# Kernel optimization log

Hardware: AMD Instinct MI355X
Metric: run time of the kernel (lower is better)

Reference implementation:

```python
import jax, jax.numpy as jnp
import numpy as np

N = 100_000   # nodes (batched over G graphs)
E = 3_200_000 # edges (avg degree 32)
G = 64        # graphs in the batch
IN_FEATS, H1, H3, NUM_CLASSES = 64, 64, 64, 2


def setup_inputs() -> dict:
    key = jax.random.key(0)
    ks = jax.random.split(key, 11)
    return {
        "in_feat": jax.random.normal(ks[0], (N, IN_FEATS), jnp.float32),
        "edge_weights": jax.random.uniform(ks[1], (E,), jnp.float32, 1e-3, 1.0),
        "W1": jax.random.normal(ks[2], (IN_FEATS, H1), jnp.float32) / np.sqrt(IN_FEATS),
        "b1": jnp.zeros((H1,), jnp.float32),
        "W2": jax.random.normal(ks[3], (H1, H3), jnp.float32) / np.sqrt(H1),
        "b2": jnp.zeros((H3,), jnp.float32),
        "Wc": jax.random.normal(ks[4], (H3, NUM_CLASSES), jnp.float32) / np.sqrt(H3),
        "bc": jnp.zeros((NUM_CLASSES,), jnp.float32),
        "edge_src": jax.random.randint(ks[5], (E,), 0, N, jnp.int32),
        "edge_dst": jax.random.randint(ks[6], (E,), 0, N, jnp.int32),
        "graph_ids": jnp.sort(jax.random.randint(ks[7], (N,), 0, G, jnp.int32)),
    }


def reference(in_feat, edge_weights, W1, b1, W2, b2, Wc, bc,
              edge_src, edge_dst, graph_ids):
    # EdgeWeightNorm(norm='right'): w_e / (sum of weights into dst(e))
    deg_w = jax.ops.segment_sum(edge_weights, edge_dst, num_segments=N)  # [N]
    nw = edge_weights / deg_w[edge_dst]                                  # [E]

    # unweighted in-degree used by SAGEConv 'gcn' aggregator
    deg = jax.ops.segment_sum(jnp.ones((E,), jnp.float32), edge_dst, num_segments=N)  # [N]

    def sage_gcn(h, W, b):
        # weighted neighbor sum: sum_e nw_e * h[src_e] scattered to dst
        msg = h[edge_src] * nw[:, None]                                  # [E, F]
        neigh = jax.ops.segment_sum(msg, edge_dst, num_segments=N)      # [N, F]
        h_neigh = (neigh + h) / (deg[:, None] + 1.0)                     # gcn: include self, /(deg+1)
        return h_neigh @ W + b                                           # fc_neigh + bias

    h = jax.nn.relu(sage_gcn(in_feat, W1, b1))
    h = jax.nn.relu(sage_gcn(h, W2, b2))

    # dgl.mean_nodes: per-graph mean of node features
    counts = jax.ops.segment_sum(jnp.ones((N,), jnp.float32), graph_ids, num_segments=G)
    hg = jax.ops.segment_sum(h, graph_ids, num_segments=G) / jnp.maximum(counts, 1.0)[:, None]

    return hg @ Wc + bc  # [G, num_classes]
```

## Files before the change

### kernel.cpp

```cpp
#include <hip/hip_runtime.h>
#include <hip/hip_fp16.h>


#define BK   1024
#define NB   128
#define CAPB 5120
#define CAPP 6144
#define SRC17 0x1FFFFu

__device__ __forceinline__ float readlane_f(float v, int l) {
    return __int_as_float(__builtin_amdgcn_readlane(__float_as_int(v), l));
}

__device__ __forceinline__ int2 ntload_i2(const int2* p) {
    unsigned long long r = __builtin_nontemporal_load((const unsigned long long*)p);
    return make_int2((int)(unsigned)(r & 0xffffffffull), (int)(unsigned)(r >> 32));
}

__device__ __forceinline__ void ntstore_f2(float2* p, float2 v) {
    union { float2 f; unsigned long long u; } c;
    c.f = v;
    __builtin_nontemporal_store(c.u, (unsigned long long*)p);
}

__global__ void k_cvt(const float4* __restrict__ x, uint2* __restrict__ xh, int n4) {
    int i = blockIdx.x * blockDim.x + threadIdx.x;
    if (i >= n4) return;
    float4 v = x[i];
    __half2 a = __floats2half2_rn(v.x, v.y);
    __half2 b = __floats2half2_rn(v.z, v.w);
    uint2 r;
    r.x = *(const unsigned*)&a;
    r.y = *(const unsigned*)&b;
    xh[i] = r;
}

__global__ __launch_bounds__(1024) void k_binB(
        const int* __restrict__ esrc, const int* __restrict__ edst,
        const float* __restrict__ ew, int* __restrict__ cursor,
        int2* __restrict__ bsw, int E, int CH) {
    __shared__ int h[BK];
    __shared__ int lcur[BK];
    const int tid = threadIdx.x;

    if (tid < BK) h[tid] = 0;
    __syncthreads();
    const int e0 = blockIdx.x * CH;
    const int e1 = min(E, e0 + CH);
    for (int e = e0 + tid; e < e1; e += 1024)
        atomicAdd(&h[edst[e] >> 7], 1);
    __syncthreads();
    if (tid < BK) {
        int c = h[tid];
        lcur[tid] = c ? atomicAdd(&cursor[tid], c) : 0;
    }
    __syncthreads();
    for (int e = e0 + tid; e < e1; e += 1024) {
        int d = edst[e];
        int b = d >> 7;
        int p = atomicAdd(&lcur[b], 1);
        if (p < CAPB)
            bsw[(size_t)b * CAPB + p] =
                make_int2(((d & 127) << 18) | esrc[e], __float_as_int(ew[e]));
    }
}

__global__ __launch_bounds__(512) void k_csrsort(
        const int2* __restrict__ bsw, const int* __restrict__ cursor,
        unsigned* __restrict__ csr, int* __restrict__ off, int* __restrict__ fill,
        int N) {
    __shared__ unsigned se[CAPP];
    __shared__ int cur[NB];
    __shared__ int pfx[NB];
    __shared__ int tot;
    const int b = blockIdx.x, tid = threadIdx.x;
    for (int i = tid; i < CAPP; i += 512) se[i] = 0u;
    if (tid < NB) cur[tid] = 0;
    __syncthreads();
    const int cnt = min(cursor[b], CAPB);
    const int2* __restrict__ eb = bsw + (size_t)b * CAPB;
    for (int i = tid; i < cnt; i += 512)
        atomicAdd(&cur[eb[i].x >> 18], 1);
    __syncthreads();
    int pc = 0;
    if (tid < NB) {
        int c0 = cur[tid & ~1], c1 = cur[tid | 1];
        pc = (max(c0, c1) + 7) & ~7;
        pfx[tid] = pc;
    }
    __syncthreads();
    for (int o = 1; o < NB; o <<= 1) {
        int t = 0;
        if (tid < NB && tid >= o) t = pfx[tid - o];
        __syncthreads();
        if (tid < NB) pfx[tid] += t;
        __syncthreads();
    }
    if (tid < NB) {
        int excl = pfx[tid] - pc;
        int node = b * NB + tid;
        if (node < N) { off[node] = b * CAPP + excl; fill[node] = cur[tid]; }
        cur[tid] = excl;
        if (tid == NB - 1) tot = min(pfx[tid], CAPP);
    }
    __syncthreads();
    for (int i = tid; i < cnt; i += 512) {
        int2 e = eb[i];
        int p = atomicAdd(&cur[e.x >> 18], 1);
        unsigned h15 = (unsigned)__half_as_ushort(
                           __float2half_rn(__int_as_float(e.y))) & 0x7FFFu;
        if (p < CAPP)
            se[p] = ((unsigned)e.x & SRC17) | (h15 << 17);
    }
    __syncthreads();
    const int T = tot;
    unsigned* __restrict__ cb = csr + (size_t)b * CAPP;
    for (int i = tid; i < T; i += 512) cb[i] = se[i];
}

__global__ void k_fill_pad(const int* __restrict__ esrc, const int* __restrict__ edst,
                           const float* __restrict__ ew, int* __restrict__ fill,
                           int2* __restrict__ csr, int E, int CAP) {
    int e = blockIdx.x * blockDim.x + threadIdx.x;
    if (e < E) {
        int d = edst[e];
        int p = atomicAdd(&fill[d], 1);
        if (p < CAP)
            csr[(size_t)d * CAP + p] = make_int2(esrc[e], __float_as_int(ew[e]));
    }
}

__global__ void k_cnt(const int* __restrict__ edst, int* __restrict__ cnt, int E) {
    int e = blockIdx.x * blockDim.x + threadIdx.x;
    if (e < E) atomicAdd(&cnt[edst[e]], 1);
}

__global__ void k_off(const int* __restrict__ cnt, int* __restrict__ off,
                      int* __restrict__ fill, int* __restrict__ cursor, int N) {
    int i    = blockIdx.x * blockDim.x + threadIdx.x;
    int lane = threadIdx.x & 63;
    int c    = (i < N) ? cnt[i] : 0;
    int pref = c;
    #pragma unroll
    for (int d = 1; d < 64; d <<= 1) {
        int t = __shfl_up(pref, d);
        if (lane >= d) pref += t;
    }
    int total = __shfl(pref, 63);
    int base  = 0;
    if (lane == 63) base = atomicAdd(cursor, total);
    base = __shfl(base, 63);
    if (i < N) {
        int p = base + pref - c;
        off[i]  = p;
        fill[i] = p;
    }
}

__global__ void k_fill(const int* __restrict__ esrc, const int* __restrict__ edst,
                       const float* __restrict__ ew, int* __restrict__ fill,
                       int2* __restrict__ csr, int E) {
    int e = blockIdx.x * blockDim.x + threadIdx.x;
    if (e < E) {
        int d = edst[e];
        int p = atomicAdd(&fill[d], 1);
        csr[p] = make_int2(esrc[e], __float_as_int(ew[e]));
    }
}

__global__ __launch_bounds__(256, 6) void k_agg_p(
        const unsigned* __restrict__ xh, const int* __restrict__ off,
        const int* __restrict__ cnt_arr, const unsigned* __restrict__ csr,
        float* __restrict__ agg, int N) {
    const int lane = threadIdx.x & 63;
    const int slot = lane >> 5;
    const int f8   = lane & 31;
    const int wq   = (blockIdx.x * blockDim.x + threadIdx.x) >> 6;
    const int nw   = (gridDim.x * blockDim.x) >> 6;
    const int npair = (N + 1) >> 1;

    for (int pr = wq; pr < npair; pr += nw) {
        const int  node  = 2 * pr + slot;
        const bool valid = node < N;
        const int  cnt_s = valid ? cnt_arr[node] : 0;
        const int  st_s  = valid ? off[node] : 0;
        const int  cA = __builtin_amdgcn_readlane(cnt_s, 0);
        const int  cB = __builtin_amdgcn_readlane(cnt_s, 32);
        const int  pc = (max(cA, cB) + 7) & ~7;

        float2 acc = {0.f, 0.f};
        float  sw  = 0.f;
        const unsigned* __restrict__ pS = csr + st_s;
        for (int k = 0; k < pc; k += 8) {
            uint4 e0 = *(const uint4*)(pS + k);
            uint4 e1 = *(const uint4*)(pS + k + 4);
            unsigned ev[8] = {e0.x, e0.y, e0.z, e0.w, e1.x, e1.y, e1.z, e1.w};
            float    w[8];
            unsigned u[8];
            #pragma unroll
            for (int t = 0; t < 8; ++t) {
                unsigned e = ev[t];
                w[t] = __half2float(__ushort_as_half((unsigned short)(e >> 17)));
                u[t] = xh[((e & SRC17) << 5) | (unsigned)f8];
            }
            #pragma unroll
            for (int t = 0; t < 8; ++t) {
                float2 v = __half22float2(*(const __half2*)&u[t]);
                acc.x = fmaf(w[t], v.x, acc.x);
                acc.y = fmaf(w[t], v.y, acc.y);
                sw += w[t];
            }
        }
        if (valid) {
            float invw = (sw > 0.f) ? (1.f / sw) : 0.f;
            float invd = 1.f / ((float)cnt_s + 1.f);
            unsigned us = xh[((unsigned)node << 5) | (unsigned)f8];
            float2 xs = __half22float2(*(const __half2*)&us);
            float2 hn;
            hn.x = (acc.x * invw + xs.x) * invd;
            hn.y = (acc.y * invw + xs.y) * invd;
            ntstore_f2(&((float2*)agg)[(size_t)node * 32 + f8], hn);
        }
    }
}

__global__ __launch_bounds__(256, 4) void k_agg_f(
        const unsigned* __restrict__ xh, const int* __restrict__ off,
        const int* __restrict__ cnt_arr, const int2* __restrict__ csr,
        float* __restrict__ agg, int N, int CAP) {
    const int lane   = threadIdx.x & 63;
    const int slot   = lane >> 5;
    const int f8     = lane & 31;
    const int wave   = (blockIdx.x * blockDim.x + threadIdx.x) >> 6;
    const int nwaves = (gridDim.x * blockDim.x) >> 6;

    int node  = wave;
    int cnt_p = 0, start_p = 0;
    if (node < N) {
        cnt_p   = cnt_arr[node];
        start_p = (CAP > 0) ? node * CAP : off[node];
        if (CAP > 0) cnt_p = min(cnt_p, CAP);
    }
    for (; node < N; node += nwaves) {
        const int cnt = cnt_p, start = start_p;
        int nn = node + nwaves;
        if (nn < N) {
            cnt_p   = cnt_arr[nn];
            start_p = (CAP > 0) ? nn * CAP : off[nn];
            if (CAP > 0) cnt_p = min(cnt_p, CAP);
        }
        int2 ee = make_int2(0, 0);
        if (lane < cnt) ee = ntload_i2(&csr[start + lane]);
        float2 acc0 = {0.f, 0.f}, acc1 = {0.f, 0.f};
        float  sw = 0.0f;
        for (int bk = 0; bk < cnt; bk += 64) {
            int   s_l = ee.x;
            float w_l = __int_as_float(ee.y);
            int2 en = make_int2(0, 0);
            int  rem = cnt - bk - 64;
            if (lane < rem) en = ntload_i2(&csr[start + bk + 64 + lane]);
            sw += w_l;
            #pragma unroll
            for (int half = 0; half < 2; ++half) {
                float    w[16];
                unsigned u[16];
                #pragma unroll
                for (int k = 0; k < 16; ++k) {
                    int idx = half * 32 + 2 * k + slot;
                    int s   = __shfl(s_l, idx);
                    w[k]    = __shfl(w_l, idx);
                    u[k]    = xh[(size_t)s * 32 + f8];
                }
                #pragma unroll
                for (int k = 0; k < 16; k += 2) {
                    float2 v0 = __half22float2(*(const __half2*)&u[k]);
                    float2 v1 = __half22float2(*(const __half2*)&u[k + 1]);
                    acc0.x = fmaf(w[k],     v0.x, acc0.x);
                    acc0.y = fmaf(w[k],     v0.y, acc0.y);
                    acc1.x = fmaf(w[k + 1], v1.x, acc1.x);
                    acc1.y = fmaf(w[k + 1], v1.y, acc1.y);
                }
            }
            ee = en;
        }
        acc0.x += acc1.x; acc0.y += acc1.y;
        acc0.x += __shfl_xor(acc0.x, 32);
        acc0.y += __shfl_xor(acc0.y, 32);
        #pragma unroll
        for (int mask = 1; mask <= 32; mask <<= 1) sw += __shfl_xor(sw, mask);
        float invw = (sw > 0.0f) ? (1.0f / sw) : 0.0f;
        float invd = 1.0f / ((float)cnt + 1.0f);
        if (lane < 32) {
            unsigned us = xh[(size_t)node * 32 + f8];
            float2 xs = __half22float2(*(const __half2*)&us);
            float2 hn;
            hn.x = (acc0.x * invw + xs.x) * invd;
            hn.y = (acc0.y * invw + xs.y) * invd;
            ntstore_f2(&((float2*)agg)[(size_t)node * 32 + f8], hn);
        }
    }
}

__global__ __launch_bounds__(256) void k_fc(
        const float* __restrict__ agg, const float* __restrict__ W,
        const float* __restrict__ b, __half* __restrict__ outh, int N) {
    const int lane   = threadIdx.x & 63;
    const int wave   = (blockIdx.x * blockDim.x + threadIdx.x) >> 6;
    const int nwaves = (gridDim.x * blockDim.x) >> 6;
    float wc[64];
    #pragma unroll
    for (int f = 0; f < 64; ++f) wc[f] = W[f * 64 + lane];
    const float bias = b[lane];
    for (int node = wave; node < N; node += nwaves) {
        float hn = agg[(size_t)node * 64 + lane];
        float o0 = bias, o1 = 0.f, o2 = 0.f, o3 = 0.f;
        #pragma unroll
        for (int f = 0; f < 64; f += 4) {
            o0 = fmaf(readlane_f(hn, f),     wc[f],     o0);
            o1 = fmaf(readlane_f(hn, f + 1), wc[f + 1], o1);
            o2 = fmaf(readlane_f(hn, f + 2), wc[f + 2], o2);
            o3 = fmaf(readlane_f(hn, f + 3), wc[f + 3], o3);
        }
        float o = fmaxf((o0 + o1) + (o2 + o3), 0.0f);
        outh[(size_t)node * 64 + lane] = __float2half_rn(o);
    }
}

__global__ __launch_bounds__(256) void k_fcpool(
        const float* __restrict__ agg, const float* __restrict__ W,
        const float* __restrict__ b, const int* __restrict__ gid,
        float* __restrict__ hg, float* __restrict__ cntg, int N) {
    const int lane   = threadIdx.x & 63;
    const int wave   = (blockIdx.x * blockDim.x + threadIdx.x) >> 6;
    const int nwaves = (gridDim.x * blockDim.x) >> 6;
    float wc[64];
    #pragma unroll
    for (int f = 0; f < 64; ++f) wc[f] = W[f * 64 + lane];
    const float bias = b[lane];
    const int per   = (N + nwaves - 1) / nwaves;
    const int start = wave * per;
    const int end   = min(N, start + per);
    if (start >= N) return;

    int   curg = -1;
    float acc  = 0.0f;
    int   c    = 0;
    for (int node = start; node < end; ++node) {
        float hn = agg[(size_t)node * 64 + lane];
        float o0 = bias, o1 = 0.f, o2 = 0.f, o3 = 0.f;
        #pragma unroll
        for (int f = 0; f < 64; f += 4) {
            o0 = fmaf(readlane_f(hn, f),     wc[f],     o0);
            o1 = fmaf(readlane_f(hn, f + 1), wc[f + 1], o1);
            o2 = fmaf(readlane_f(hn, f + 2), wc[f + 2], o2);
            o3 = fmaf(readlane_f(hn, f + 3), wc[f + 3], o3);
        }
        float o = fmaxf((o0 + o1) + (o2 + o3), 0.0f);
        int g = gid[node];
        if (g != curg) {
            if (c > 0) {
                atomicAdd(&hg[curg * 64 + lane], acc);
                if (lane == 0) atomicAdd(&cntg[curg], (float)c);
            }
            curg = g; acc = 0.0f; c = 0;
        }
        acc += o;
        ++c;
    }
    if (c > 0) {
        atomicAdd(&hg[curg * 64 + lane], acc);
        if (lane == 0) atomicAdd(&cntg[curg], (float)c);
    }
}

__global__ void k_out(const float* __restrict__ hg, const float* __restrict__ cntg,
                      const float* __restrict__ Wc, const float* __restrict__ bc,
                      float* __restrict__ out, int G) {
    int t = blockIdx.x * blockDim.x + threadIdx.x;
    if (t >= G * 2) return;
    int g = t >> 1, c = t & 1;
    float ct = fmaxf(cntg[g], 1.0f);
    float o  = bc[c];
    for (int f = 0; f < 64; ++f)
        o += (hg[g * 64 + f] / ct) * Wc[f * 2 + c];
    out[t] = o;
}

extern "C" void kernel_launch(void* const* d_in, const int* in_sizes, int n_in,
                              void* d_out, int out_size, void* d_ws, size_t ws_size,
                              hipStream_t stream) {
    const float* in_feat = (const float*)d_in[0];
    const float* ew      = (const float*)d_in[1];
    const float* W1      = (const float*)d_in[2];
    const float* b1      = (const float*)d_in[3];
    const float* W2      = (const float*)d_in[4];
    const float* b2      = (const float*)d_in[5];
    const float* Wc      = (const float*)d_in[6];
    const float* bc      = (const float*)d_in[7];
    const int*   esrc    = (const int*)d_in[8];
    const int*   edst    = (const int*)d_in[9];
    const int*   gid     = (const int*)d_in[10];

    const int E = in_sizes[1];
    const int N = in_sizes[10];
    const int G = out_size / 2;
    float* outp = (float*)d_out;

    auto alignup = [](size_t x) { return (x + 15) & ~(size_t)15; };
    char* base = (char*)d_ws;
    const int FC_BLK = 1024, AGG_BLK = 2048;
    const int n4 = N * 16;

    const int B   = (N + NB - 1) / NB;
    const int CHB = (E + 255) / 256;

    size_t zhdr  = ((size_t)G * 64 + G + BK) * 4;
    size_t o_off = alignup(zhdr);
    size_t o_fil = o_off + alignup((size_t)N * 4);
    size_t o_bsw = o_fil + alignup((size_t)N * 4);
    size_t o_csr = o_bsw + alignup((size_t)B * CAPB * 8);
    size_t o_t1  = o_csr + alignup((size_t)B * CAPP * 4);
    size_t o_t2  = o_t1 + alignup((size_t)N * 64 * 4);
    size_t o_xh  = o_t2 + alignup((size_t)N * 64 * 4);
    size_t o_th  = o_xh + alignup((size_t)N * 64 * 2);
    size_t needB = o_th + (size_t)N * 64 * 2;

    bool cap_ok = ((size_t)E / B) + 512 < CAPB && N <= (1 << 17);

    if (ws_size >= needB && B <= BK && cap_ok) {
        float*    hg     = (float*)base;
        float*    cntg   = hg + (size_t)G * 64;
        int*      cursor = (int*)(cntg + G);
        int*      off    = (int*)(base + o_off);
        int*      fill   = (int*)(base + o_fil);
        int2*     bsw    = (int2*)(base + o_bsw);
        unsigned* csr    = (unsigned*)(base + o_csr);
        float*    t1     = (float*)(base + o_t1);
        float*    t2     = (float*)(base + o_t2);
        unsigned* xh0    = (unsigned*)(base + o_xh);
        __half*   th1    = (__half*)(base + o_th);

        hipMemsetAsync(d_ws, 0, zhdr, stream);
        k_cvt    <<<(n4 + 255) / 256, 256, 0, stream>>>((const float4*)in_feat, (uint2*)xh0, n4);
        k_binB   <<<256, 1024, 0, stream>>>(esrc, edst, ew, cursor, bsw, E, CHB);
        k_csrsort<<<B, 512, 0, stream>>>(bsw, cursor, csr, off, fill, N);
        k_agg_p <<<AGG_BLK, 256, 0, stream>>>(xh0, off, fill, csr, t1, N);
        k_fc    <<<FC_BLK, 256, 0, stream>>>(t1, W1, b1, th1, N);
        k_agg_p <<<AGG_BLK, 256, 0, stream>>>((const unsigned*)th1, off, fill, csr, t2, N);
        k_fcpool<<<FC_BLK, 256, 0, stream>>>(t2, W2, b2, gid, hg, cntg, N);
        k_out   <<<1, 128, 0, stream>>>(hg, cntg, Wc, bc, outp, G);
        return;
    }

    const int CAP = 96;
    size_t hdr    = ((size_t)G * 64 + G + 1 + N) * 4;
    size_t needB2 = alignup(hdr) + alignup((size_t)N * CAP * 8)
                  + alignup((size_t)N * 64 * 4) * 2
                  + alignup((size_t)N * 64 * 2) * 2;
    if (ws_size >= needB2) {
        size_t o = 0;
        float* hg     = (float*)(base + o);
        float* cntg   = hg + (size_t)G * 64;
        int*   fill   = (int*)(cntg + G) + 1;
        o += alignup(hdr);
        int2*     csr = (int2*)(base + o);    o += alignup((size_t)N * CAP * 8);
        float*    t1  = (float*)(base + o);   o += alignup((size_t)N * 64 * 4);
        float*    t2  = (float*)(base + o);   o += alignup((size_t)N * 64 * 4);
        unsigned* xh0 = (unsigned*)(base + o); o += alignup((size_t)N * 64 * 2);
        __half*   th1 = (__half*)(base + o);

        hipMemsetAsync(d_ws, 0, hdr, stream);
        k_cvt     <<<(n4 + 255) / 256, 256, 0, stream>>>((const float4*)in_feat, (uint2*)xh0, n4);
        k_fill_pad<<<(E + 255) / 256, 256, 0, stream>>>(esrc, edst, ew, fill, csr, E, CAP);
        k_agg_f <<<AGG_BLK, 256, 0, stream>>>(xh0, (const int*)nullptr, fill, csr, t1, N, CAP);
        k_fc    <<<FC_BLK, 256, 0, stream>>>(t1, W1, b1, th1, N);
        k_agg_f <<<AGG_BLK, 256, 0, stream>>>((const unsigned*)th1, (const int*)nullptr, fill, csr, t2, N, CAP);
        k_fcpool<<<FC_BLK, 256, 0, stream>>>(t2, W2, b2, gid, hg, cntg, N);
        k_out   <<<1, 128, 0, stream>>>(hg, cntg, Wc, bc, outp, G);
        return;
    }

    {
        size_t o = 0;
        float* hg     = (float*)(base + o);
        float* cntg   = hg + (size_t)G * 64;
        int*   cursor = (int*)(cntg + G);
        int*   cnt    = cursor + 1;
        o += alignup(hdr);
        int*      off  = (int*)(base + o);    o += alignup((size_t)N * 4);
        int*      fill = (int*)(base + o);    o += alignup((size_t)N * 4);
        int2*     csr  = (int2*)(base + o);   o += alignup((size_t)E * 8);
        float*    t1   = (float*)(base + o);  o += alignup((size_t)N * 64 * 4);
        float*    t2   = (float*)(base + o);  o += alignup((size_t)N * 64 * 4);
        unsigned* xh0  = (unsigned*)(base + o); o += alignup((size_t)N * 64 * 2);
        __half*   th1  = (__half*)(base + o);

        hipMemsetAsync(d_ws, 0, hdr, stream);
        k_cvt <<<(n4 + 255) / 256, 256, 0, stream>>>((const float4*)in_feat, (uint2*)xh0, n4);
        k_cnt <<<(E + 255) / 256, 256, 0, stream>>>(edst, cnt, E);
        k_off <<<(N + 255) / 256, 256, 0, stream>>>(cnt, off, fill, cursor, N);
        k_fill<<<(E + 255) / 256, 256, 0, stream>>>(esrc, edst, ew, fill, csr, E);
        k_agg_f <<<AGG_BLK, 256, 0, stream>>>(xh0, off, cnt, csr, t1, N, 0);
        k_fc    <<<FC_BLK, 256, 0, stream>>>(t1, W1, b1, th1, N);
        k_agg_f <<<AGG_BLK, 256, 0, stream>>>((const unsigned*)th1, off, cnt, csr, t2, N, 0);
        k_fcpool<<<FC_BLK, 256, 0, stream>>>(t2, W2, b2, gid, hg, cntg, N);
        k_out   <<<1, 128, 0, stream>>>(hg, cntg, Wc, bc, outp, G);
    }
}
```

Measured before the change: 375.0 us.

## Fuse neighbor aggregation with dense layer and pooling per node block

Replaces the separate aggregation and FC kernels with two fused kernels. Each block aggregates 128 nodes into shared memory and then applies the 64x64 linear layer (plus ReLU, or plus the per-graph mean-pool atomics in layer two) directly. This removes the fp32 t1/t2 intermediate round trips through global memory and two kernel launches. In exchange, each block holds a 32KB shared tile and a 64-register weight column, which cuts occupancy for the latency-bound gather phase and removes the grid-stride load balancing.

```diff
diff --git a/kernel.cpp b/kernel.cpp
--- a/kernel.cpp
+++ b/kernel.cpp
@@ -118,71 +118,25 @@
     for (int i = tid; i < T; i += 512) cb[i] = se[i];
 }
 
-__global__ void k_fill_pad(const int* __restrict__ esrc, const int* __restrict__ edst,
-                           const float* __restrict__ ew, int* __restrict__ fill,
-                           int2* __restrict__ csr, int E, int CAP) {
-    int e = blockIdx.x * blockDim.x + threadIdx.x;
-    if (e < E) {
-        int d = edst[e];
-        int p = atomicAdd(&fill[d], 1);
-        if (p < CAP)
-            csr[(size_t)d * CAP + p] = make_int2(esrc[e], __float_as_int(ew[e]));
-    }
-}
-
-__global__ void k_cnt(const int* __restrict__ edst, int* __restrict__ cnt, int E) {
-    int e = blockIdx.x * blockDim.x + threadIdx.x;
-    if (e < E) atomicAdd(&cnt[edst[e]], 1);
-}
-
-__global__ void k_off(const int* __restrict__ cnt, int* __restrict__ off,
-                      int* __restrict__ fill, int* __restrict__ cursor, int N) {
-    int i    = blockIdx.x * blockDim.x + threadIdx.x;
-    int lane = threadIdx.x & 63;
-    int c    = (i < N) ? cnt[i] : 0;
-    int pref = c;
-    #pragma unroll
-    for (int d = 1; d < 64; d <<= 1) {
-        int t = __shfl_up(pref, d);
-        if (lane >= d) pref += t;
-    }
-    int total = __shfl(pref, 63);
-    int base  = 0;
-    if (lane == 63) base = atomicAdd(cursor, total);
-    base = __shfl(base, 63);
-    if (i < N) {
-        int p = base + pref - c;
-        off[i]  = p;
-        fill[i] = p;
-    }
-}
-
-__global__ void k_fill(const int* __restrict__ esrc, const int* __restrict__ edst,
-                       const float* __restrict__ ew, int* __restrict__ fill,
-                       int2* __restrict__ csr, int E) {
-    int e = blockIdx.x * blockDim.x + threadIdx.x;
-    if (e < E) {
-        int d = edst[e];
-        int p = atomicAdd(&fill[d], 1);
-        csr[p] = make_int2(esrc[e], __float_as_int(ew[e]));
-    }
-}
-
-__global__ __launch_bounds__(256, 6) void k_agg_p(
+
+__global__ __launch_bounds__(256, 4) void k_aggfc1(
         const unsigned* __restrict__ xh, const int* __restrict__ off,
-        const int* __restrict__ cnt_arr, const unsigned* __restrict__ csr,
-        float* __restrict__ agg, int N) {
-    const int lane = threadIdx.x & 63;
+        const int* __restrict__ fill, const unsigned* __restrict__ csr,
+        const float* __restrict__ W, const float* __restrict__ bias,
+        __half* __restrict__ outh, int N) {
+    __shared__ float hn[NB * 64];
+    const int tid  = threadIdx.x;
+    const int b    = blockIdx.x;
+    const int lane = tid & 63;
     const int slot = lane >> 5;
     const int f8   = lane & 31;
-    const int wq   = (blockIdx.x * blockDim.x + threadIdx.x) >> 6;
-    const int nw   = (gridDim.x * blockDim.x) >> 6;
-    const int npair = (N + 1) >> 1;
-
-    for (int pr = wq; pr < npair; pr += nw) {
-        const int  node  = 2 * pr + slot;
+    const int wv   = tid >> 6;
+    const int node0 = b * NB;
+
+    for (int pq = wv; pq < 64; pq += 4) {
+        const int  node  = node0 + 2 * pq + slot;
         const bool valid = node < N;
-        const int  cnt_s = valid ? cnt_arr[node] : 0;
+        const int  cnt_s = valid ? fill[node] : 0;
         const int  st_s  = valid ? off[node] : 0;
         const int  cA = __builtin_amdgcn_readlane(cnt_s, 0);
         const int  cB = __builtin_amdgcn_readlane(cnt_s, 32);
@@ -216,11 +170,181 @@
             float invd = 1.f / ((float)cnt_s + 1.f);
             unsigned us = xh[((unsigned)node << 5) | (unsigned)f8];
             float2 xs = __half22float2(*(const __half2*)&us);
-            float2 hn;
-            hn.x = (acc.x * invw + xs.x) * invd;
-            hn.y = (acc.y * invw + xs.y) * invd;
-            ntstore_f2(&((float2*)agg)[(size_t)node * 32 + f8], hn);
-        }
+            int r = 2 * pq + slot;
+            hn[r * 64 + f8 * 2    ] = (acc.x * invw + xs.x) * invd;
+            hn[r * 64 + f8 * 2 + 1] = (acc.y * invw + xs.y) * invd;
+        }
+    }
+    __syncthreads();
+
+    float wc[64];
+    #pragma unroll
+    for (int f = 0; f < 64; ++f) wc[f] = W[f * 64 + lane];
+    const float bb = bias[lane];
+    for (int r = wv; r < NB; r += 4) {
+        int node = node0 + r;
+        if (node >= N) continue;
+        const float4* __restrict__ row = (const float4*)&hn[r * 64];
+        float o = bb;
+        #pragma unroll
+        for (int q = 0; q < 16; ++q) {
+            float4 h4 = row[q];
+            o = fmaf(h4.x, wc[4 * q    ], o);
+            o = fmaf(h4.y, wc[4 * q + 1], o);
+            o = fmaf(h4.z, wc[4 * q + 2], o);
+            o = fmaf(h4.w, wc[4 * q + 3], o);
+        }
+        o = fmaxf(o, 0.f);
+        outh[(size_t)node * 64 + lane] = __float2half_rn(o);
+    }
+}
+
+__global__ __launch_bounds__(256, 4) void k_aggfc2(
+        const unsigned* __restrict__ xh, const int* __restrict__ off,
+        const int* __restrict__ fill, const unsigned* __restrict__ csr,
+        const float* __restrict__ W, const float* __restrict__ bias,
+        const int* __restrict__ gid, float* __restrict__ hg,
+        float* __restrict__ cntg, int N) {
+    __shared__ float hn[NB * 64];
+    const int tid  = threadIdx.x;
+    const int b    = blockIdx.x;
+    const int lane = tid & 63;
+    const int slot = lane >> 5;
+    const int f8   = lane & 31;
+    const int wv   = tid >> 6;
+    const int node0 = b * NB;
+
+    for (int pq = wv; pq < 64; pq += 4) {
+        const int  node  = node0 + 2 * pq + slot;
+        const bool valid = node < N;
+        const int  cnt_s = valid ? fill[node] : 0;
+        const int  st_s  = valid ? off[node] : 0;
+        const int  cA = __builtin_amdgcn_readlane(cnt_s, 0);
+        const int  cB = __builtin_amdgcn_readlane(cnt_s, 32);
+        const int  pc = (max(cA, cB) + 7) & ~7;
+
+        float2 acc = {0.f, 0.f};
+        float  sw  = 0.f;
+        const unsigned* __restrict__ pS = csr + st_s;
+        for (int k = 0; k < pc; k += 8) {
+            uint4 e0 = *(const uint4*)(pS + k);
+            uint4 e1 = *(const uint4*)(pS + k + 4);
+            unsigned ev[8] = {e0.x, e0.y, e0.z, e0.w, e1.x, e1.y, e1.z, e1.w};
+            float    w[8];
+            unsigned u[8];
+            #pragma unroll
+            for (int t = 0; t < 8; ++t) {
+                unsigned e = ev[t];
+                w[t] = __half2float(__ushort_as_half((unsigned short)(e >> 17)));
+                u[t] = xh[((e & SRC17) << 5) | (unsigned)f8];
+            }
+            #pragma unroll
+            for (int t = 0; t < 8; ++t) {
+                float2 v = __half22float2(*(const __half2*)&u[t]);
+                acc.x = fmaf(w[t], v.x, acc.x);
+                acc.y = fmaf(w[t], v.y, acc.y);
+                sw += w[t];
+            }
+        }
+        if (valid) {
+            float invw = (sw > 0.f) ? (1.f / sw) : 0.f;
+            float invd = 1.f / ((float)cnt_s + 1.f);
+            unsigned us = xh[((unsigned)node << 5) | (unsigned)f8];
+            float2 xs = __half22float2(*(const __half2*)&us);
+            int r = 2 * pq + slot;
+            hn[r * 64 + f8 * 2    ] = (acc.x * invw + xs.x) * invd;
+            hn[r * 64 + f8 * 2 + 1] = (acc.y * invw + xs.y) * invd;
+        }
+    }
+    __syncthreads();
+
+    float wc[64];
+    #pragma unroll
+    for (int f = 0; f < 64; ++f) wc[f] = W[f * 64 + lane];
+    const float bb = bias[lane];
+
+    int   curg = -1;
+    float acc  = 0.f;
+    int   c    = 0;
+    const int r0 = wv * 32, r1 = r0 + 32;
+    for (int r = r0; r < r1; ++r) {
+        int node = node0 + r;
+        if (node >= N) break;
+        const float4* __restrict__ row = (const float4*)&hn[r * 64];
+        float o = bb;
+        #pragma unroll
+        for (int q = 0; q < 16; ++q) {
+            float4 h4 = row[q];
+            o = fmaf(h4.x, wc[4 * q    ], o);
+            o = fmaf(h4.y, wc[4 * q + 1], o);
+            o = fmaf(h4.z, wc[4 * q + 2], o);
+            o = fmaf(h4.w, wc[4 * q + 3], o);
+        }
+        o = fmaxf(o, 0.f);
+        int g = gid[node];
+        if (g != curg) {
+            if (c > 0) {
+                atomicAdd(&hg[curg * 64 + lane], acc);
+                if (lane == 0) atomicAdd(&cntg[curg], (float)c);
+            }
+            curg = g; acc = 0.f; c = 0;
+        }
+        acc += o;
+        ++c;
+    }
+    if (c > 0) {
+        atomicAdd(&hg[curg * 64 + lane], acc);
+        if (lane == 0) atomicAdd(&cntg[curg], (float)c);
+    }
+}
+
+__global__ void k_fill_pad(const int* __restrict__ esrc, const int* __restrict__ edst,
+                           const float* __restrict__ ew, int* __restrict__ fill,
+                           int2* __restrict__ csr, int E, int CAP) {
+    int e = blockIdx.x * blockDim.x + threadIdx.x;
+    if (e < E) {
+        int d = edst[e];
+        int p = atomicAdd(&fill[d], 1);
+        if (p < CAP)
+            csr[(size_t)d * CAP + p] = make_int2(esrc[e], __float_as_int(ew[e]));
+    }
+}
+
+__global__ void k_cnt(const int* __restrict__ edst, int* __restrict__ cnt, int E) {
+    int e = blockIdx.x * blockDim.x + threadIdx.x;
+    if (e < E) atomicAdd(&cnt[edst[e]], 1);
+}
+
+__global__ void k_off(const int* __restrict__ cnt, int* __restrict__ off,
+                      int* __restrict__ fill, int* __restrict__ cursor, int N) {
+    int i    = blockIdx.x * blockDim.x + threadIdx.x;
+    int lane = threadIdx.x & 63;
+    int c    = (i < N) ? cnt[i] : 0;
+    int pref = c;
+    #pragma unroll
+    for (int d = 1; d < 64; d <<= 1) {
+        int t = __shfl_up(pref, d);
+        if (lane >= d) pref += t;
+    }
+    int total = __shfl(pref, 63);
+    int base  = 0;
+    if (lane == 63) base = atomicAdd(cursor, total);
+    base = __shfl(base, 63);
+    if (i < N) {
+        int p = base + pref - c;
+        off[i]  = p;
+        fill[i] = p;
+    }
+}
+
+__global__ void k_fill(const int* __restrict__ esrc, const int* __restrict__ edst,
+                       const float* __restrict__ ew, int* __restrict__ fill,
+                       int2* __restrict__ csr, int E) {
+    int e = blockIdx.x * blockDim.x + threadIdx.x;
+    if (e < E) {
+        int d = edst[e];
+        int p = atomicAdd(&fill[d], 1);
+        csr[p] = make_int2(esrc[e], __float_as_int(ew[e]));
     }
 }
 
@@ -419,9 +543,7 @@
     size_t o_fil = o_off + alignup((size_t)N * 4);
     size_t o_bsw = o_fil + alignup((size_t)N * 4);
     size_t o_csr = o_bsw + alignup((size_t)B * CAPB * 8);
-    size_t o_t1  = o_csr + alignup((size_t)B * CAPP * 4);
-    size_t o_t2  = o_t1 + alignup((size_t)N * 64 * 4);
-    size_t o_xh  = o_t2 + alignup((size_t)N * 64 * 4);
+    size_t o_xh  = o_csr + alignup((size_t)B * CAPP * 4);
     size_t o_th  = o_xh + alignup((size_t)N * 64 * 2);
     size_t needB = o_th + (size_t)N * 64 * 2;
 
@@ -435,8 +557,6 @@
         int*      fill   = (int*)(base + o_fil);
         int2*     bsw    = (int2*)(base + o_bsw);
         unsigned* csr    = (unsigned*)(base + o_csr);
-        float*    t1     = (float*)(base + o_t1);
-        float*    t2     = (float*)(base + o_t2);
         unsigned* xh0    = (unsigned*)(base + o_xh);
         __half*   th1    = (__half*)(base + o_th);
 
@@ -444,11 +564,10 @@
         k_cvt    <<<(n4 + 255) / 256, 256, 0, stream>>>((const float4*)in_feat, (uint2*)xh0, n4);
         k_binB   <<<256, 1024, 0, stream>>>(esrc, edst, ew, cursor, bsw, E, CHB);
         k_csrsort<<<B, 512, 0, stream>>>(bsw, cursor, csr, off, fill, N);
-        k_agg_p <<<AGG_BLK, 256, 0, stream>>>(xh0, off, fill, csr, t1, N);
-        k_fc    <<<FC_BLK, 256, 0, stream>>>(t1, W1, b1, th1, N);
-        k_agg_p <<<AGG_BLK, 256, 0, stream>>>((const unsigned*)th1, off, fill, csr, t2, N);
-        k_fcpool<<<FC_BLK, 256, 0, stream>>>(t2, W2, b2, gid, hg, cntg, N);
-        k_out   <<<1, 128, 0, stream>>>(hg, cntg, Wc, bc, outp, G);
+        k_aggfc1 <<<B, 256, 0, stream>>>(xh0, off, fill, csr, W1, b1, th1, N);
+        k_aggfc2 <<<B, 256, 0, stream>>>((const unsigned*)th1, off, fill, csr,
+                                         W2, b2, gid, hg, cntg, N);
+        k_out    <<<1, 128, 0, stream>>>(hg, cntg, Wc, bc, outp, G);
         return;
     }
 
```

New measurement: 423.6 us. +13.0%, slower.
